# Performance work log

Hardware: AMD Instinct MI355X
Metric: run time of the kernel (lower is better)

The kernel has to match this reference:

```python
import jax, jax.numpy as jnp
import numpy as np

BS, NCAMS, CIN, H, W = 4, 1, 256, 56, 200
MID = 128
DCH = 112  # (58-2)/0.5 depth bins
GX, GY, GZ = 128, 128, 16  # voxel grid


def setup_inputs() -> dict:
    key = jax.random.key(0)
    ks = jax.random.split(key, 32)
    f32 = jnp.float32

    def n(k, shape, scale=0.05):
        return jax.random.normal(k, shape, f32) * scale

    inp = {
        'img_feat': jax.random.normal(ks[0], (BS, NCAMS, CIN, H, W), f32),
        'scaled_pixel_size': jax.random.uniform(ks[1], (BS * NCAMS, 1), f32) * 2.0 + 0.5,
        # normalized sampling coords, slightly beyond [-1,1] to exercise zero padding
        'grids': jax.random.uniform(ks[2], (NCAMS, BS, GX, GY, GZ, 3), f32) * 2.2 - 1.1,
        # reduce_conv: Conv2d(CIN->MID,3x3,bias) + BN(affine, eval=per-channel scale/shift)
        'rc_w': n(ks[3], (MID, CIN, 3, 3)),
        'rc_b': n(ks[4], (MID,)),
        'rc_s': 1.0 + n(ks[5], (MID,)),
        'rc_t': n(ks[6], (MID,)),
        # Mlp(1 -> MID -> MID)
        'fc1_w': n(ks[7], (MID, 1), 0.5),
        'fc1_b': n(ks[8], (MID,)),
        'fc2_w': n(ks[9], (MID, MID)),
        'fc2_b': n(ks[10], (MID,)),
        # SELayer 1x1 convs (act on [N,MID,1,1] -> plain linears)
        'se_rw': n(ks[11], (MID, MID)),
        'se_rb': n(ks[12], (MID,)),
        'se_ew': n(ks[13], (MID, MID)),
        'se_eb': n(ks[14], (MID,)),
        # 3 BasicBlocks: conv3x3(no bias)+BN+ReLU+conv3x3(no bias)+BN, residual, ReLU
        'bb_w1': n(ks[15], (3, MID, MID, 3, 3)),
        'bb_s1': 1.0 + n(ks[16], (3, MID)),
        'bb_t1': n(ks[17], (3, MID)),
        'bb_w2': n(ks[18], (3, MID, MID, 3, 3)),
        'bb_s2': 1.0 + n(ks[19], (3, MID)),
        'bb_t2': n(ks[20], (3, MID)),
        # depth_pred 1x1 conv MID -> DCH
        'dp_w': n(ks[21], (DCH, MID)),
        'dp_b': n(ks[22], (DCH,)),
    }
    return inp


def _conv2d(x, w):
    return jax.lax.conv_general_dilated(x, w, (1, 1), 'SAME',
                                        dimension_numbers=('NCHW', 'OIHW', 'NCHW'))


def _aff(x, s, t):
    return x * s[None, :, None, None] + t[None, :, None, None]


def grid_sample_3d(feat, grid):
    """Trilinear grid_sample, zeros padding, align_corners=False.
    feat: [N,C,D,H,W]; grid: [N,X,Y,Z,3] with (x,y,z) in [-1,1] indexing (W,H,D).
    Returns [N,C,X,Y,Z]."""
    N, C, D, Hh, Ww = feat.shape
    ix = (grid[..., 0] + 1.0) * (Ww * 0.5) - 0.5
    iy = (grid[..., 1] + 1.0) * (Hh * 0.5) - 0.5
    iz = (grid[..., 2] + 1.0) * (D * 0.5) - 0.5
    x0 = jnp.floor(ix); y0 = jnp.floor(iy); z0 = jnp.floor(iz)
    fx, fy, fz = ix - x0, iy - y0, iz - z0

    def one(f, x0, y0, z0, fx, fy, fz):
        out = jnp.zeros((C,) + x0.shape, f.dtype)
        x0i = x0.astype(jnp.int32); y0i = y0.astype(jnp.int32); z0i = z0.astype(jnp.int32)
        for dz in (0, 1):
            for dy in (0, 1):
                for dx in (0, 1):
                    xi = x0i + dx; yi = y0i + dy; zi = z0i + dz
                    wgt = ((fx if dx else 1.0 - fx) * (fy if dy else 1.0 - fy)
                           * (fz if dz else 1.0 - fz))
                    valid = ((xi >= 0) & (xi < Ww) & (yi >= 0) & (yi < Hh)
                             & (zi >= 0) & (zi < D))
                    v = f[:, jnp.clip(zi, 0, D - 1), jnp.clip(yi, 0, Hh - 1),
                          jnp.clip(xi, 0, Ww - 1)]
                    out = out + v * (wgt * valid)[None]
        return out

    return jax.vmap(one)(feat, x0, y0, z0, fx, fy, fz)


def reference(img_feat, scaled_pixel_size, grids, rc_w, rc_b, rc_s, rc_t,
              fc1_w, fc1_b, fc2_w, fc2_b, se_rw, se_rb, se_ew, se_eb,
              bb_w1, bb_s1, bb_t1, bb_w2, bb_s2, bb_t2, dp_w, dp_b):
    bs, n_cams, c, h, w = img_feat.shape
    x = img_feat.reshape(bs * n_cams, c, h, w)
    # DepthNet (infer_mode): reduce_conv
    x = jax.nn.relu(_aff(_conv2d(x, rc_w) + rc_b[None, :, None, None], rc_s, rc_t))
    # Mlp on scaled_pixel_size + SE gating
    hmid = jax.nn.relu(scaled_pixel_size @ fc1_w.T + fc1_b) @ fc2_w.T + fc2_b
    se = jax.nn.relu(hmid @ se_rw.T + se_rb) @ se_ew.T + se_eb
    x = x * jax.nn.sigmoid(se)[:, :, None, None]
    # 3 BasicBlocks
    for i in range(3):
        y = jax.nn.relu(_aff(_conv2d(x, bb_w1[i]), bb_s1[i], bb_t1[i]))
        y = _aff(_conv2d(y, bb_w2[i]), bb_s2[i], bb_t2[i])
        x = jax.nn.relu(x + y)
    # depth_pred 1x1 conv, softmax over depth bins
    depth_feat = jnp.einsum('nchw,dc->ndhw', x, dp_w) + dp_b[None, :, None, None]
    depth = jax.nn.softmax(depth_feat, axis=1)
    depth = depth.reshape(bs, n_cams, 1, DCH, h, w)
    # per-camera frustum -> voxel bilinear sampling
    all_voxel_features = []
    for i in range(n_cams):
        all_voxel_features.append(grid_sample_3d(depth[:, i], grids[i]))
    agg = all_voxel_features[0]  # n_cams == 1 path in original forward
    return agg  # [bs, 1, GX, GY, GZ]
```

## Files before the change

kernel.cpp:

```cpp
#include <hip/hip_runtime.h>
#include <math.h>

typedef _Float16 v8h __attribute__((ext_vector_type(8)));
typedef float v4f __attribute__((ext_vector_type(4)));
typedef float v16f __attribute__((ext_vector_type(16)));

__global__ void __launch_bounds__(256) prep_repack_kernel(
    const float* __restrict__ rc_w, const float* __restrict__ bb_w1,
    const float* __restrict__ bb_w2, const float* __restrict__ dp_w,
    const float* __restrict__ sps,
    const float* __restrict__ fc1_w, const float* __restrict__ fc1_b,
    const float* __restrict__ fc2_w, const float* __restrict__ fc2_b,
    const float* __restrict__ se_rw, const float* __restrict__ se_rb,
    const float* __restrict__ se_ew, const float* __restrict__ se_eb,
    _Float16* __restrict__ wrc, _Float16* __restrict__ wbb,
    _Float16* __restrict__ wdp, float* __restrict__ sig) {
  const int bx = blockIdx.x;
  const int tid = threadIdx.x;
  __shared__ float lds[9224];

  if (bx < 32) {
    const float* src = rc_w + (size_t)bx * 4 * 2304;
#pragma unroll
    for (int r = 0; r < 36; ++r) {
      int e = r * 256 + tid;
      int col = e / 2304;
      int rem = e - col * 2304;
      lds[col * 2305 + rem] = src[e];
    }
    __syncthreads();
#pragma unroll
    for (int ro = 0; ro < 5; ++ro) {
      int lidx = ro * 256 + tid;
      if (lidx < 1152) {
        int col = lidx & 3;
        int r = lidx >> 2;
        int kh = r & 1;
        int ct = r >> 1;
        int tap = ct % 9, c16 = ct / 9;
        v8h o;
#pragma unroll
        for (int j = 0; j < 8; ++j)
          o[j] = (_Float16)lds[col * 2305 + (c16 * 16 + kh * 8 + j) * 9 + tap];
        *(v8h*)(wrc + ((size_t)r * 128 + bx * 4 + col) * 8) = o;
      }
    }
  } else if (bx < 128) {
    const int t = bx - 32;
    const int k = t >> 4, g = t & 15;
    const float* base = (k < 3) ? (bb_w1 + (size_t)k * 147456)
                                : (bb_w2 + (size_t)(k - 3) * 147456);
    const int cslot = (k < 3) ? (2 * k) : (2 * (k - 3) + 1);
    const float* src = base + (size_t)g * 8 * 1152;
#pragma unroll
    for (int r = 0; r < 36; ++r) {
      int e = r * 256 + tid;
      int col = e / 1152;
      int rem = e - col * 1152;
      lds[col * 1153 + rem] = src[e];
    }
    __syncthreads();
#pragma unroll
    for (int ro = 0; ro < 5; ++ro) {
      int lidx = ro * 256 + tid;
      if (lidx < 1152) {
        int col = lidx & 7;
        int r = lidx >> 3;
        int kh = r & 1;
        int ct = r >> 1;
        int tap = ct % 9, c16 = ct / 9;
        v8h o;
#pragma unroll
        for (int j = 0; j < 8; ++j)
          o[j] = (_Float16)lds[col * 1153 + (c16 * 16 + kh * 8 + j) * 9 + tap];
        *(v8h*)(wbb + (size_t)cslot * 147456 + ((size_t)r * 128 + g * 8 + col) * 8) = o;
      }
    }
  } else if (bx < 135) {
    int s3 = (bx - 128) * 256 + tid;
    v8h o;
#pragma unroll
    for (int j = 0; j < 8; ++j) o[j] = (_Float16)dp_w[(size_t)s3 * 8 + j];
    *(v8h*)(wdp + (size_t)s3 * 8) = o;
  } else {
    const int j = tid;
    const bool on = j < 128;
    for (int b = 0; b < 4; ++b) {
      float h1 = 0.f;
      if (on) h1 = fmaxf(sps[b] * fc1_w[j] + fc1_b[j], 0.f);
      __syncthreads();
      if (on) lds[j] = h1;
      __syncthreads();
      float hm = 0.f;
      if (on) {
        hm = fc2_b[j];
        for (int k = 0; k < 128; ++k) hm += lds[k] * fc2_w[j * 128 + k];
      }
      __syncthreads();
      if (on) lds[j] = hm;
      __syncthreads();
      float t = 0.f;
      if (on) {
        t = se_rb[j];
        for (int k = 0; k < 128; ++k) t += lds[k] * se_rw[j * 128 + k];
        t = fmaxf(t, 0.f);
      }
      __syncthreads();
      if (on) lds[j] = t;
      __syncthreads();
      if (on) {
        float se = se_eb[j];
        for (int k = 0; k < 128; ++k) se += lds[k] * se_ew[j * 128 + k];
        sig[b * 128 + j] = 1.f / (1.f + expf(-se));
      }
      __syncthreads();
    }
  }
}

__global__ void __launch_bounds__(256) convert_kernel(
    const float* __restrict__ img, _Float16* __restrict__ act16) {
  const int i = blockIdx.x * 256 + threadIdx.x;
  const int cq = blockIdx.y;
  const int n = i / 11200;
  const int hw = i - n * 11200;
  const float* ip = img + (size_t)n * 2867200 + (size_t)(cq * 64) * 11200 + hw;
  float v[64];
#pragma unroll
  for (int k = 0; k < 64; ++k) v[k] = ip[(size_t)k * 11200];
  _Float16* op = act16 + (size_t)i * 256 + cq * 64;
#pragma unroll
  for (int g = 0; g < 8; ++g) {
    v8h o;
#pragma unroll
    for (int j = 0; j < 8; ++j) o[j] = (_Float16)v[g * 8 + j];
    *(v8h*)(op + g * 8) = o;
  }
}

template <int CIN, int MODE>
__global__ void __launch_bounds__(512, 4) conv3x3_kernel(
    const _Float16* __restrict__ act, const _Float16* __restrict__ wr,
    const _Float16* __restrict__ xprev, const float* __restrict__ bias,
    const float* __restrict__ sc, const float* __restrict__ tr,
    const float* __restrict__ sig_se, _Float16* __restrict__ out) {
  constexpr int NCH = CIN / 16;
  const int wt = blockIdx.x, ht = blockIdx.y;
  const int n = blockIdx.z >> 1, cg = blockIdx.z & 1;
  const int h0 = ht * 8, w0 = wt * 32;
  const int tid = threadIdx.x;
  const int wave = tid >> 6, lane = tid & 63;
  const int l31 = lane & 31, khalf = lane >> 5;
  const int wv = wave >> 1, kc = wave & 1;

  __shared__ alignas(16) _Float16 ldsA[2][2 * 340 * 8];
  __shared__ alignas(16) _Float16 ldsB[2][1152 * 8];

  size_t goffA[2];
  int loffA[2];
  bool exA[2], okA[2];
#pragma unroll
  for (int it = 0; it < 2; ++it) {
    int slot = it * 512 + tid;
    int pos = slot >> 1, part = slot & 1;
    int hh = pos / 34, ww = pos - hh * 34;
    int gh = h0 - 1 + hh, gw = w0 - 1 + ww;
    exA[it] = slot < 680;
    bool inimg = (unsigned)gh < 56u && (unsigned)gw < 200u;
    okA[it] = exA[it] && inimg;
    loffA[it] = (part * 340 + pos) * 8;
    int ghc = okA[it] ? gh : 0, gwc = okA[it] ? gw : 0;
    goffA[it] = (((size_t)n * 56 + ghc) * 200 + gwc) * CIN + part * 8;
  }
  size_t goffB[3];
  int loffB[3];
  bool exB[3];
#pragma unroll
  for (int it = 0; it < 3; ++it) {
    int slot = it * 512 + tid;
    exB[it] = slot < 1152;
    int s = exB[it] ? slot : 0;
    int tap = s >> 7, kh = (s >> 6) & 1, co = s & 63;
    goffB[it] = (((size_t)(tap * 2 + kh)) * 128 + cg * 64 + co) * 8;
    loffB[it] = s * 8;
  }

  const v8h zero8 = {(_Float16)0, (_Float16)0, (_Float16)0, (_Float16)0,
                     (_Float16)0, (_Float16)0, (_Float16)0, (_Float16)0};
  v8h preA[2], preB[3];
#pragma unroll
  for (int it = 0; it < 2; ++it) preA[it] = okA[it] ? *(const v8h*)(act + goffA[it]) : zero8;
#pragma unroll
  for (int it = 0; it < 3; ++it) preB[it] = exB[it] ? *(const v8h*)(wr + goffB[it]) : zero8;

  v16f acc[2];
#pragma unroll
  for (int mt = 0; mt < 2; ++mt)
#pragma unroll
    for (int r = 0; r < 16; ++r) acc[mt][r] = 0.f;

#pragma unroll 1
  for (int c = 0; c < NCH; ++c) {
    _Float16* aB = &ldsA[c & 1][0];
    _Float16* bB = &ldsB[c & 1][0];
#pragma unroll
    for (int it = 0; it < 2; ++it)
      if (exA[it]) *(v8h*)(aB + loffA[it]) = preA[it];
#pragma unroll
    for (int it = 0; it < 3; ++it)
      if (exB[it]) *(v8h*)(bB + loffB[it]) = preB[it];
    __syncthreads();
    if (c + 1 < NCH) {
#pragma unroll
      for (int it = 0; it < 2; ++it)
        preA[it] = okA[it] ? *(const v8h*)(act + goffA[it] + (size_t)(c + 1) * 16) : zero8;
#pragma unroll
      for (int it = 0; it < 3; ++it)
        preB[it] = exB[it] ? *(const v8h*)(wr + goffB[it] + (size_t)(c + 1) * 18432) : zero8;
    }
#pragma unroll
    for (int dy = 0; dy < 3; ++dy) {
#pragma unroll
      for (int dx = 0; dx < 3; ++dx) {
        const int tap = dy * 3 + dx;
        v8h bfrag = *(const v8h*)(bB + (tap * 128 + khalf * 64 + kc * 32 + l31) * 8);
#pragma unroll
        for (int mt = 0; mt < 2; ++mt) {
          const int pos = (wv * 2 + mt + dy) * 34 + l31 + dx;
          v8h afrag = *(const v8h*)(aB + (khalf * 340 + pos) * 8);
          acc[mt] = __builtin_amdgcn_mfma_f32_32x32x16_f16(afrag, bfrag, acc[mt], 0, 0, 0);
        }
      }
    }
  }

#pragma unroll
  for (int mt = 0; mt < 2; ++mt) {
    const int h = h0 + wv * 2 + mt;
    const int cc = cg * 64 + kc * 32 + l31;
    const float s = sc[cc], t = tr[cc];
    float bb = 0.f, sg = 1.f;
    if constexpr (MODE == 0) {
      bb = bias[cc];
      sg = sig_se[n * 128 + cc];
    }
#pragma unroll
    for (int r = 0; r < 16; ++r) {
      const int m = (r & 3) + 8 * (r >> 2) + 4 * khalf;
      const int w = w0 + m;
      if (w < 200) {
        float v = acc[mt][r];
        size_t oidx = (((size_t)n * 56 + h) * 200 + w) * 128 + cc;
        if constexpr (MODE == 0) v = fmaxf((v + bb) * s + t, 0.f) * sg;
        if constexpr (MODE == 1) v = fmaxf(v * s + t, 0.f);
        if constexpr (MODE == 2) v = fmaxf((float)xprev[oidx] + v * s + t, 0.f);
        out[oidx] = (_Float16)v;
      }
    }
  }
}

__global__ void __launch_bounds__(256) depth_proj_softmax_kernel(
    const _Float16* __restrict__ x, const _Float16* __restrict__ wdp,
    const float* __restrict__ dp_b, _Float16* __restrict__ depth) {
  const int wave = threadIdx.x >> 6, lane = threadIdx.x & 63;
  const int q = lane >> 4, l16 = lane & 15;
  const int pos0 = blockIdx.x * 64 + wave * 16;

  v4f acc[7];
#pragma unroll
  for (int nt = 0; nt < 7; ++nt) {
    float bv = dp_b[nt * 16 + l16];
    acc[nt] = {bv, bv, bv, bv};
  }
#pragma unroll
  for (int c0 = 0; c0 < 128; c0 += 32) {
    v8h a = *(const v8h*)(x + (size_t)(pos0 + l16) * 128 + c0 + q * 8);
#pragma unroll
    for (int nt = 0; nt < 7; ++nt) {
      v8h b = *(const v8h*)(wdp + (size_t)(nt * 16 + l16) * 128 + c0 + q * 8);
      acc[nt] = __builtin_amdgcn_mfma_f32_16x16x32_f16(a, b, acc[nt], 0, 0, 0);
    }
  }
  float m[4];
#pragma unroll
  for (int r = 0; r < 4; ++r) {
    m[r] = acc[0][r];
#pragma unroll
    for (int nt = 1; nt < 7; ++nt) m[r] = fmaxf(m[r], acc[nt][r]);
  }
#pragma unroll
  for (int off = 1; off < 16; off <<= 1)
#pragma unroll
    for (int r = 0; r < 4; ++r) m[r] = fmaxf(m[r], __shfl_xor(m[r], off));
  float s[4] = {0.f, 0.f, 0.f, 0.f};
#pragma unroll
  for (int nt = 0; nt < 7; ++nt)
#pragma unroll
    for (int r = 0; r < 4; ++r) {
      float e = expf(acc[nt][r] - m[r]);
      acc[nt][r] = e;
      s[r] += e;
    }
#pragma unroll
  for (int off = 1; off < 16; off <<= 1)
#pragma unroll
    for (int r = 0; r < 4; ++r) s[r] += __shfl_xor(s[r], off);
#pragma unroll
  for (int r = 0; r < 4; ++r) {
    const float inv = 1.f / s[r];
    const size_t p = pos0 + q * 4 + r;
#pragma unroll
    for (int nt = 0; nt < 7; ++nt)
      depth[p * 112 + nt * 16 + l16] = (_Float16)(acc[nt][r] * inv);
  }
}

__global__ void __launch_bounds__(256) gridsample_kernel(
    const float* __restrict__ grids, const _Float16* __restrict__ depth,
    float* __restrict__ out) {
  const int i = blockIdx.x * 256 + threadIdx.x;
  const int n = i >> 18;
  const float gx = grids[(size_t)i * 3];
  const float gy = grids[(size_t)i * 3 + 1];
  const float gz = grids[(size_t)i * 3 + 2];
  const float ix = (gx + 1.f) * 100.f - 0.5f;
  const float iy = (gy + 1.f) * 28.f - 0.5f;
  const float iz = (gz + 1.f) * 56.f - 0.5f;
  const float xf = floorf(ix), yf = floorf(iy), zf = floorf(iz);
  const int x0 = (int)xf, y0 = (int)yf, z0 = (int)zf;
  const float fx = ix - xf, fy = iy - yf, fz = iz - zf;
  const bool zv0 = (unsigned)z0 < 112u;
  const bool zv1 = (unsigned)(z0 + 1) < 112u;
  const float wz0 = 1.f - fz, wz1 = fz;
  float acc = 0.f;
#pragma unroll
  for (int dy = 0; dy < 2; ++dy) {
    const int yi = y0 + dy;
    const float wy = dy ? fy : 1.f - fy;
#pragma unroll
    for (int dx = 0; dx < 2; ++dx) {
      const int xi = x0 + dx;
      const float wx = dx ? fx : 1.f - fx;
      if ((unsigned)xi < 200u && (unsigned)yi < 56u) {
        const _Float16* bp = depth + ((size_t)n * 11200 + yi * 200 + xi) * 112;
        float v0 = zv0 ? (float)bp[z0] : 0.f;
        float v1 = zv1 ? (float)bp[z0 + 1] : 0.f;
        acc += (wx * wy) * (wz0 * v0 + wz1 * v1);
      }
    }
  }
  out[i] = acc;
}

extern "C" void kernel_launch(void* const* d_in, const int* in_sizes, int n_in,
                              void* d_out, int out_size, void* d_ws, size_t ws_size,
                              hipStream_t stream) {
  (void)in_sizes; (void)n_in; (void)out_size; (void)ws_size;
  const float* img = (const float*)d_in[0];
  const float* sps = (const float*)d_in[1];
  const float* grids = (const float*)d_in[2];
  const float* rc_w = (const float*)d_in[3];
  const float* rc_b = (const float*)d_in[4];
  const float* rc_s = (const float*)d_in[5];
  const float* rc_t = (const float*)d_in[6];
  const float* fc1_w = (const float*)d_in[7];
  const float* fc1_b = (const float*)d_in[8];
  const float* fc2_w = (const float*)d_in[9];
  const float* fc2_b = (const float*)d_in[10];
  const float* se_rw = (const float*)d_in[11];
  const float* se_rb = (const float*)d_in[12];
  const float* se_ew = (const float*)d_in[13];
  const float* se_eb = (const float*)d_in[14];
  const float* bb_w1 = (const float*)d_in[15];
  const float* bb_s1 = (const float*)d_in[16];
  const float* bb_t1 = (const float*)d_in[17];
  const float* bb_w2 = (const float*)d_in[18];
  const float* bb_s2 = (const float*)d_in[19];
  const float* bb_t2 = (const float*)d_in[20];
  const float* dp_w = (const float*)d_in[21];
  const float* dp_b = (const float*)d_in[22];
  float* outp = (float*)d_out;

  char* ws = (char*)d_ws;
  _Float16* act16 = (_Float16*)(ws + 0);
  _Float16* depth16 = (_Float16*)(ws + 0);
  _Float16* xa = (_Float16*)(ws + 23068672);
  _Float16* xb = (_Float16*)(ws + 23068672 + 11534336);
  _Float16* yb = (_Float16*)(ws + 23068672 + 2 * 11534336);
  _Float16* wrc = (_Float16*)(ws + 57671680);
  _Float16* wdp = (_Float16*)(ws + 57671680 + 589824);
  _Float16* wbb = (_Float16*)(ws + 58327040);
  float* sig = (float*)(ws + 58327040 + 1769472);

  prep_repack_kernel<<<dim3(136), 256, 0, stream>>>(
      rc_w, bb_w1, bb_w2, dp_w, sps, fc1_w, fc1_b, fc2_w, fc2_b, se_rw, se_rb,
      se_ew, se_eb, wrc, wbb, wdp, sig);
  convert_kernel<<<dim3(175, 4), 256, 0, stream>>>(img, act16);

  dim3 cgrid(7, 7, 8);
  conv3x3_kernel<256, 0><<<cgrid, 512, 0, stream>>>(act16, wrc, nullptr, rc_b, rc_s,
                                                    rc_t, sig, xa);
  _Float16* xcur = xa;
  _Float16* xnxt = xb;
  for (int i = 0; i < 3; ++i) {
    conv3x3_kernel<128, 1><<<cgrid, 512, 0, stream>>>(
        xcur, wbb + (size_t)(2 * i) * 147456, nullptr, nullptr, bb_s1 + i * 128,
        bb_t1 + i * 128, nullptr, yb);
    conv3x3_kernel<128, 2><<<cgrid, 512, 0, stream>>>(
        yb, wbb + (size_t)(2 * i + 1) * 147456, xcur, nullptr, bb_s2 + i * 128,
        bb_t2 + i * 128, nullptr, xnxt);
    _Float16* t = xcur;
    xcur = xnxt;
    xnxt = t;
  }

  depth_proj_softmax_kernel<<<dim3(700), 256, 0, stream>>>(xcur, wdp, dp_b, depth16);
  gridsample_kernel<<<dim3(4096), 256, 0, stream>>>(grids, depth16, outp);
}
```

Before: 421.7 us.

## Deepen conv prefetch to two chunks and reuse A fragments across dy

The conv3x3 main loop is unrolled by two with separate register prefetch sets, so global loads are issued two chunks ahead of the MFMA work. The tap loops are reordered to iterate dx outer, loading four A rows per dx and reusing them across dy, which cuts LDS fragment reads per chunk. The weight-repack prep kernel is also split into twice as many smaller blocks with half the shared memory. Extra prefetch registers may raise register pressure and lower occupancy, and the loop assumes an even chunk count.

```diff
diff --git a/kernel.cpp b/kernel.cpp
--- a/kernel.cpp
+++ b/kernel.cpp
@@ -17,12 +17,12 @@
     _Float16* __restrict__ wdp, float* __restrict__ sig) {
   const int bx = blockIdx.x;
   const int tid = threadIdx.x;
-  __shared__ float lds[9224];
-
-  if (bx < 32) {
-    const float* src = rc_w + (size_t)bx * 4 * 2304;
-#pragma unroll
-    for (int r = 0; r < 36; ++r) {
+  __shared__ float lds[4612];
+
+  if (bx < 64) {
+    const float* src = rc_w + (size_t)bx * 2 * 2304;
+#pragma unroll
+    for (int r = 0; r < 18; ++r) {
       int e = r * 256 + tid;
       int col = e / 2304;
       int rem = e - col * 2304;
@@ -30,9 +30,40 @@
     }
     __syncthreads();
 #pragma unroll
-    for (int ro = 0; ro < 5; ++ro) {
+    for (int ro = 0; ro < 3; ++ro) {
       int lidx = ro * 256 + tid;
-      if (lidx < 1152) {
+      if (lidx < 576) {
+        int col = lidx & 1;
+        int r = lidx >> 1;
+        int kh = r & 1;
+        int ct = r >> 1;
+        int tap = ct % 9, c16 = ct / 9;
+        v8h o;
+#pragma unroll
+        for (int j = 0; j < 8; ++j)
+          o[j] = (_Float16)lds[col * 2305 + (c16 * 16 + kh * 8 + j) * 9 + tap];
+        *(v8h*)(wrc + ((size_t)r * 128 + bx * 2 + col) * 8) = o;
+      }
+    }
+  } else if (bx < 256) {
+    const int t = bx - 64;
+    const int k = t >> 5, g = t & 31;
+    const float* base = (k < 3) ? (bb_w1 + (size_t)k * 147456)
+                                : (bb_w2 + (size_t)(k - 3) * 147456);
+    const int cslot = (k < 3) ? (2 * k) : (2 * (k - 3) + 1);
+    const float* src = base + (size_t)g * 4 * 1152;
+#pragma unroll
+    for (int r = 0; r < 18; ++r) {
+      int e = r * 256 + tid;
+      int col = e / 1152;
+      int rem = e - col * 1152;
+      lds[col * 1153 + rem] = src[e];
+    }
+    __syncthreads();
+#pragma unroll
+    for (int ro = 0; ro < 3; ++ro) {
+      int lidx = ro * 256 + tid;
+      if (lidx < 576) {
         int col = lidx & 3;
         int r = lidx >> 2;
         int kh = r & 1;
@@ -41,43 +72,12 @@
         v8h o;
 #pragma unroll
         for (int j = 0; j < 8; ++j)
-          o[j] = (_Float16)lds[col * 2305 + (c16 * 16 + kh * 8 + j) * 9 + tap];
-        *(v8h*)(wrc + ((size_t)r * 128 + bx * 4 + col) * 8) = o;
-      }
-    }
-  } else if (bx < 128) {
-    const int t = bx - 32;
-    const int k = t >> 4, g = t & 15;
-    const float* base = (k < 3) ? (bb_w1 + (size_t)k * 147456)
-                                : (bb_w2 + (size_t)(k - 3) * 147456);
-    const int cslot = (k < 3) ? (2 * k) : (2 * (k - 3) + 1);
-    const float* src = base + (size_t)g * 8 * 1152;
-#pragma unroll
-    for (int r = 0; r < 36; ++r) {
-      int e = r * 256 + tid;
-      int col = e / 1152;
-      int rem = e - col * 1152;
-      lds[col * 1153 + rem] = src[e];
-    }
-    __syncthreads();
-#pragma unroll
-    for (int ro = 0; ro < 5; ++ro) {
-      int lidx = ro * 256 + tid;
-      if (lidx < 1152) {
-        int col = lidx & 7;
-        int r = lidx >> 3;
-        int kh = r & 1;
-        int ct = r >> 1;
-        int tap = ct % 9, c16 = ct / 9;
-        v8h o;
-#pragma unroll
-        for (int j = 0; j < 8; ++j)
           o[j] = (_Float16)lds[col * 1153 + (c16 * 16 + kh * 8 + j) * 9 + tap];
-        *(v8h*)(wbb + (size_t)cslot * 147456 + ((size_t)r * 128 + g * 8 + col) * 8) = o;
-      }
-    }
-  } else if (bx < 135) {
-    int s3 = (bx - 128) * 256 + tid;
+        *(v8h*)(wbb + (size_t)cslot * 147456 + ((size_t)r * 128 + g * 4 + col) * 8) = o;
+      }
+    }
+  } else if (bx < 263) {
+    int s3 = (bx - 256) * 256 + tid;
     v8h o;
 #pragma unroll
     for (int j = 0; j < 8; ++j) o[j] = (_Float16)dp_w[(size_t)s3 * 8 + j];
@@ -187,11 +187,17 @@
 
   const v8h zero8 = {(_Float16)0, (_Float16)0, (_Float16)0, (_Float16)0,
                      (_Float16)0, (_Float16)0, (_Float16)0, (_Float16)0};
-  v8h preA[2], preB[3];
-#pragma unroll
-  for (int it = 0; it < 2; ++it) preA[it] = okA[it] ? *(const v8h*)(act + goffA[it]) : zero8;
-#pragma unroll
-  for (int it = 0; it < 3; ++it) preB[it] = exB[it] ? *(const v8h*)(wr + goffB[it]) : zero8;
+  v8h preA0[2], preB0[3], preA1[2], preB1[3];
+#pragma unroll
+  for (int it = 0; it < 2; ++it) {
+    preA0[it] = okA[it] ? *(const v8h*)(act + goffA[it]) : zero8;
+    preA1[it] = okA[it] ? *(const v8h*)(act + goffA[it] + 16) : zero8;
+  }
+#pragma unroll
+  for (int it = 0; it < 3; ++it) {
+    preB0[it] = exB[it] ? *(const v8h*)(wr + goffB[it]) : zero8;
+    preB1[it] = exB[it] ? *(const v8h*)(wr + goffB[it] + 18432) : zero8;
+  }
 
   v16f acc[2];
 #pragma unroll
@@ -199,39 +205,57 @@
 #pragma unroll
     for (int r = 0; r < 16; ++r) acc[mt][r] = 0.f;
 
+  auto compute = [&](const _Float16* aB, const _Float16* bB) {
+#pragma unroll
+    for (int dx = 0; dx < 3; ++dx) {
+      v8h a[4];
+#pragma unroll
+      for (int r = 0; r < 4; ++r)
+        a[r] = *(const v8h*)(aB + (khalf * 340 + (wv * 2 + r) * 34 + l31 + dx) * 8);
+#pragma unroll
+      for (int dy = 0; dy < 3; ++dy) {
+        v8h bf = *(const v8h*)(bB + ((dy * 3 + dx) * 128 + khalf * 64 + kc * 32 + l31) * 8);
+        acc[0] = __builtin_amdgcn_mfma_f32_32x32x16_f16(a[dy], bf, acc[0], 0, 0, 0);
+        acc[1] = __builtin_amdgcn_mfma_f32_32x32x16_f16(a[dy + 1], bf, acc[1], 0, 0, 0);
+      }
+    }
+  };
+
 #pragma unroll 1
-  for (int c = 0; c < NCH; ++c) {
-    _Float16* aB = &ldsA[c & 1][0];
-    _Float16* bB = &ldsB[c & 1][0];
+  for (int c = 0; c < NCH; c += 2) {
 #pragma unroll
     for (int it = 0; it < 2; ++it)
-      if (exA[it]) *(v8h*)(aB + loffA[it]) = preA[it];
+      if (exA[it]) *(v8h*)(&ldsA[0][0] + loffA[it]) = preA0[it];
 #pragma unroll
     for (int it = 0; it < 3; ++it)
-      if (exB[it]) *(v8h*)(bB + loffB[it]) = preB[it];
+      if (exB[it]) *(v8h*)(&ldsB[0][0] + loffB[it]) = preB0[it];
+    if (c + 2 < NCH) {
+#pragma unroll
+      for (int it = 0; it < 2; ++it)
+        preA0[it] = okA[it] ? *(const v8h*)(act + goffA[it] + (size_t)(c + 2) * 16) : zero8;
+#pragma unroll
+      for (int it = 0; it < 3; ++it)
+        preB0[it] = exB[it] ? *(const v8h*)(wr + goffB[it] + (size_t)(c + 2) * 18432) : zero8;
+    }
     __syncthreads();
-    if (c + 1 < NCH) {
+    compute(&ldsA[0][0], &ldsB[0][0]);
+
+#pragma unroll
+    for (int it = 0; it < 2; ++it)
+      if (exA[it]) *(v8h*)(&ldsA[1][0] + loffA[it]) = preA1[it];
+#pragma unroll
+    for (int it = 0; it < 3; ++it)
+      if (exB[it]) *(v8h*)(&ldsB[1][0] + loffB[it]) = preB1[it];
+    if (c + 3 < NCH) {
 #pragma unroll
       for (int it = 0; it < 2; ++it)
-        preA[it] = okA[it] ? *(const v8h*)(act + goffA[it] + (size_t)(c + 1) * 16) : zero8;
+        preA1[it] = okA[it] ? *(const v8h*)(act + goffA[it] + (size_t)(c + 3) * 16) : zero8;
 #pragma unroll
       for (int it = 0; it < 3; ++it)
-        preB[it] = exB[it] ? *(const v8h*)(wr + goffB[it] + (size_t)(c + 1) * 18432) : zero8;
-    }
-#pragma unroll
-    for (int dy = 0; dy < 3; ++dy) {
-#pragma unroll
-      for (int dx = 0; dx < 3; ++dx) {
-        const int tap = dy * 3 + dx;
-        v8h bfrag = *(const v8h*)(bB + (tap * 128 + khalf * 64 + kc * 32 + l31) * 8);
-#pragma unroll
-        for (int mt = 0; mt < 2; ++mt) {
-          const int pos = (wv * 2 + mt + dy) * 34 + l31 + dx;
-          v8h afrag = *(const v8h*)(aB + (khalf * 340 + pos) * 8);
-          acc[mt] = __builtin_amdgcn_mfma_f32_32x32x16_f16(afrag, bfrag, acc[mt], 0, 0, 0);
-        }
-      }
-    }
+        preB1[it] = exB[it] ? *(const v8h*)(wr + goffB[it] + (size_t)(c + 3) * 18432) : zero8;
+    }
+    __syncthreads();
+    compute(&ldsA[1][0], &ldsB[1][0]);
   }
 
 #pragma unroll
@@ -393,7 +417,7 @@
   _Float16* wbb = (_Float16*)(ws + 58327040);
   float* sig = (float*)(ws + 58327040 + 1769472);
 
-  prep_repack_kernel<<<dim3(136), 256, 0, stream>>>(
+  prep_repack_kernel<<<dim3(264), 256, 0, stream>>>(
       rc_w, bb_w1, bb_w2, dp_w, sps, fc1_w, fc1_b, fc2_w, fc2_b, se_rw, se_rb,
       se_ew, se_eb, wrc, wbb, wdp, sig);
   convert_kernel<<<dim3(175, 4), 256, 0, stream>>>(img, act16);
```

Measured after the change: 417.6 us. No clear change (-1.0%).
